# Kernel tuning notes

Measured on AMD Instinct MI355X. Metric: run time of the kernel, lower is better.

## Reference

```python
import jax, jax.numpy as jnp
import numpy as np

N_NODES = 25000
N_EDGES = 400000
EMBED_DIM = 128
NUM_HEADS = 8
D_K = EMBED_DIM // NUM_HEADS


def setup_inputs() -> dict:
    key = jax.random.key(0)
    ks = jax.random.split(key, 8)
    sc = 1.0 / np.sqrt(EMBED_DIM)
    return {
        "x": jax.random.normal(ks[0], (N_NODES, EMBED_DIM), jnp.float32),
        "edge_index": jax.random.randint(ks[1], (2, N_EDGES), 0, N_NODES),
        "attn_bias": jax.random.normal(ks[2], (N_EDGES, NUM_HEADS), jnp.float32),
        "Wq": jax.random.normal(ks[3], (EMBED_DIM, EMBED_DIM), jnp.float32) * sc,
        "bq": jnp.zeros((EMBED_DIM,), jnp.float32),
        "Wk": jax.random.normal(ks[4], (EMBED_DIM, EMBED_DIM), jnp.float32) * sc,
        "bk": jnp.zeros((EMBED_DIM,), jnp.float32),
        "Wv": jax.random.normal(ks[5], (EMBED_DIM, EMBED_DIM), jnp.float32) * sc,
        "bv": jnp.zeros((EMBED_DIM,), jnp.float32),
        "Wo": jax.random.normal(ks[6], (EMBED_DIM, EMBED_DIM), jnp.float32) * sc,
        "bo": jnp.zeros((EMBED_DIM,), jnp.float32),
    }


def reference(x, edge_index, attn_bias, Wq, bq, Wk, bk, Wv, bv, Wo, bo):
    N = x.shape[0]
    E = edge_index.shape[1]
    H, dk = NUM_HEADS, D_K
    scale = 1.0 / np.sqrt(dk).astype(np.float32)
    dst = edge_index[0]  # query/aggregation node per edge
    src = edge_index[1]  # key/value node per edge

    # project at node level (as torch: linear(x)[index]), then gather per edge
    q = (x @ Wq.T + bq)[dst].reshape(E, H, dk)
    k = (x @ Wk.T + bk)[src].reshape(E, H, dk)
    v = (x @ Wv.T + bv)[src].reshape(E, H, dk)

    logits = scale * jnp.sum(q * k, axis=2) + attn_bias  # [E, H]

    # segment softmax over edges grouped by destination node
    m = jax.ops.segment_max(logits, dst, num_segments=N)     # [N, H]
    e = jnp.exp(logits - m[dst])                              # [E, H]
    z = jax.ops.segment_sum(e, dst, num_segments=N)           # [N, H]
    scores = e / z[dst]                                       # [E, H]

    agg = jax.ops.segment_sum(scores[..., None] * v, dst, num_segments=N)  # [N, H, dk]
    out = agg.reshape(N, H * dk) @ Wo.T + bo                   # [N, embed_dim]
    return out, logits[..., None]
```

## Files before the change

kernel.cpp:

```cpp
#include <hip/hip_runtime.h>
#include <math.h>

#define N_NODES 25000
#define N_EDGES 400000
#define EMBED   128
#define HEADS   8
#define DK      16
#define MAXDEG  96
#define NX (N_NODES * 128)
#define GBLK 391
#define SCAT_BLK 391
#define TOT_BLK (3 * GBLK + SCAT_BLK)

typedef __attribute__((ext_vector_type(8))) short bf16x8;
typedef __attribute__((ext_vector_type(4))) float f32x4;
typedef unsigned int uint;
typedef unsigned short ushort;

__device__ inline uint pack2_bf16(float a, float b) {
    union { float f; uint u; } ua, ub;
    ua.f = a; ub.f = b;
    uint ra = (ua.u + 0x7FFFu + ((ua.u >> 16) & 1u)) >> 16;
    uint rb = (ub.u + 0x7FFFu + ((ub.u >> 16) & 1u)) >> 16;
    return (ra & 0xFFFFu) | (rb << 16);
}
__device__ inline ushort cvt_bf16(float a) {
    union { float f; uint u; } ua; ua.f = a;
    return (ushort)((ua.u + 0x7FFFu + ((ua.u >> 16) & 1u)) >> 16);
}
__device__ inline float bf16_lo(uint u) {
    union { uint u; float f; } x; x.u = u << 16; return x.f;
}
__device__ inline float bf16_hi(uint u) {
    union { uint u; float f; } x; x.u = u & 0xFFFF0000u; return x.f;
}

__global__ __launch_bounds__(256) void prep(
    const float* __restrict__ Wq, const float* __restrict__ Wk,
    const float* __restrict__ Wv, const float* __restrict__ Wo,
    ushort* __restrict__ wb, int* __restrict__ deg)
{
    int i = blockIdx.x * 256 + threadIdx.x;
    if (i < N_NODES) deg[i] = 0;
    if (i < 32768) {
        int j = i * 2;
        const float* src = (j < 16384) ? Wq + j
                         : (j < 32768) ? Wk + (j - 16384)
                         : (j < 49152) ? Wv + (j - 32768)
                         :               Wo + (j - 49152);
        float2 v = *reinterpret_cast<const float2*>(src);
        reinterpret_cast<uint*>(wb)[i] = pack2_bf16(v.x, v.y);
    }
}

__global__ __launch_bounds__(256) void gemm_qkv_scatter(
    const float* __restrict__ x, const ushort* __restrict__ Wall,
    const float* __restrict__ bq, const float* __restrict__ bk,
    const float* __restrict__ bv,
    ushort* __restrict__ Qb, ushort* __restrict__ Kb, ushort* __restrict__ Vb,
    const int* __restrict__ ei, int* __restrict__ deg, int2* __restrict__ csr2)
{
    const int bx = blockIdx.x;
    if ((bx & 3) == 3) {
        int t = (bx >> 2) * 256 + threadIdx.x;
        int e = t * 4;
        if (e < N_EDGES) {
            int4 d = *reinterpret_cast<const int4*>(ei + e);
            int4 s = *reinterpret_cast<const int4*>(ei + N_EDGES + e);
            int p0 = atomicAdd(&deg[d.x], 1);
            if (p0 < MAXDEG) csr2[d.x * MAXDEG + p0] = make_int2(e, s.x);
            int p1 = atomicAdd(&deg[d.y], 1);
            if (p1 < MAXDEG) csr2[d.y * MAXDEG + p1] = make_int2(e + 1, s.y);
            int p2 = atomicAdd(&deg[d.z], 1);
            if (p2 < MAXDEG) csr2[d.z * MAXDEG + p2] = make_int2(e + 2, s.z);
            int p3 = atomicAdd(&deg[d.w], 1);
            if (p3 < MAXDEG) csr2[d.w * MAXDEG + p3] = make_int2(e + 3, s.w);
        }
        return;
    }

    const int gi    = (bx >> 2) * 3 + (bx & 3);
    const int which = gi / GBLK;
    const int mb    = gi - which * GBLK;
    const ushort* W = Wall + which * 16384;
    const float* bias = (which == 0) ? bq : (which == 1) ? bk : bv;
    ushort* C = (which == 0) ? Qb : (which == 1) ? Kb : Vb;

    const int lane = threadIdx.x & 63;
    const int wave = threadIdx.x >> 6;
    const int ml   = lane & 15;
    const int quad = lane >> 4;
    const int m0   = mb * 64 + wave * 16;

    int arow = m0 + ml; if (arow >= N_NODES) arow = N_NODES - 1;
    const float* xp = x + arow * 128 + quad * 8;

    bf16x8 af[4];
#pragma unroll
    for (int ks = 0; ks < 4; ++ks) {
        float4 a0 = *reinterpret_cast<const float4*>(xp + ks * 32);
        float4 a1 = *reinterpret_cast<const float4*>(xp + ks * 32 + 4);
        uint* u = reinterpret_cast<uint*>(&af[ks]);
        u[0] = pack2_bf16(a0.x, a0.y); u[1] = pack2_bf16(a0.z, a0.w);
        u[2] = pack2_bf16(a1.x, a1.y); u[3] = pack2_bf16(a1.z, a1.w);
    }

    f32x4 acc[8];
#pragma unroll
    for (int ct = 0; ct < 8; ++ct) acc[ct] = (f32x4){0.f, 0.f, 0.f, 0.f};

#pragma unroll
    for (int ks = 0; ks < 4; ++ks) {
#pragma unroll
        for (int ct = 0; ct < 8; ++ct) {
            bf16x8 bf = *reinterpret_cast<const bf16x8*>(
                W + (ct * 16 + ml) * 128 + ks * 32 + quad * 8);
            acc[ct] = __builtin_amdgcn_mfma_f32_16x16x32_bf16(af[ks], bf, acc[ct], 0, 0, 0);
        }
    }

#pragma unroll
    for (int ct = 0; ct < 8; ++ct) {
        int col = ct * 16 + ml;
        float b = bias[col];
#pragma unroll
        for (int r = 0; r < 4; ++r) {
            int row = m0 + quad * 4 + r;
            if (row < N_NODES)
                C[row * 128 + col] = cvt_bf16(acc[ct][r] + b);
        }
    }
}

__global__ __launch_bounds__(256) void fused_attn_out(
    const ushort* __restrict__ Q2, const ushort* __restrict__ K2,
    const ushort* __restrict__ V2,
    const float* __restrict__ attn_bias,
    const int* __restrict__ deg, const int2* __restrict__ csr2,
    const ushort* __restrict__ Wo2, const float* __restrict__ bo,
    float* __restrict__ logits, float* __restrict__ out)
{
    __shared__ ushort agg_sh[16 * 136];

    const int tid  = threadIdx.x;
    const int lane = tid & 63;
    const int wid  = tid >> 6;
    const int n0 = blockIdx.x * 4;
    const int n  = n0 + wid;
    int dg = deg[n]; if (dg > MAXDEG) dg = MAXDEG;
    const int start = n * MAXDEG;
    const int h  = lane & 7;
    const int es = lane >> 3;
    const int ml   = lane & 15;
    const int quad = lane >> 4;

    if (tid < 204)
        *reinterpret_cast<uint4*>(reinterpret_cast<char*>(agg_sh) + 1088 + tid * 16) =
            make_uint4(0u, 0u, 0u, 0u);

    const uint4* Qu4 = reinterpret_cast<const uint4*>(Q2);
    const uint4* Ku4 = reinterpret_cast<const uint4*>(K2);
    const uint4* Vu4 = reinterpret_cast<const uint4*>(V2);

    uint4 qa = Qu4[n * 16 + h * 2];
    uint4 qb = Qu4[n * 16 + h * 2 + 1];
    float qf[16];
    {
        uint qq[8] = {qa.x, qa.y, qa.z, qa.w, qb.x, qb.y, qb.z, qb.w};
#pragma unroll
        for (int j = 0; j < 8; ++j) {
            qf[2 * j]     = bf16_lo(qq[j]);
            qf[2 * j + 1] = bf16_hi(qq[j]);
        }
    }

    float acc[16];
#pragma unroll
    for (int j = 0; j < 16; ++j) acc[j] = 0.f;
    float z = 0.f;

    if (dg > 0) {
        int2 ep = csr2[start + (es < dg ? es : dg - 1)];
        for (int base = 0; base < dg; base += 8) {
            int e = ep.x, s = ep.y;
            bool valid = (base + es) < dg;

            uint4 k0 = Ku4[s * 16 + h * 2];
            uint4 k1 = Ku4[s * 16 + h * 2 + 1];
            uint4 v0 = Vu4[s * 16 + h * 2];
            uint4 v1 = Vu4[s * 16 + h * 2 + 1];
            float bias = attn_bias[e * 8 + h];

            int nb = base + 8;
            if (nb < dg) {
                int t2 = nb + es; if (t2 >= dg) t2 = dg - 1;
                ep = csr2[start + t2];
            }

            uint kk[8] = {k0.x, k0.y, k0.z, k0.w, k1.x, k1.y, k1.z, k1.w};
            float d = 0.f;
#pragma unroll
            for (int j = 0; j < 8; ++j)
                d += qf[2 * j] * bf16_lo(kk[j]) + qf[2 * j + 1] * bf16_hi(kk[j]);

            float l = 0.25f * d + bias;
            float p = 0.f;
            if (valid) {
                __builtin_nontemporal_store(l, &logits[e * 8 + h]);
                p = __expf(l);
            }
            z += p;

            uint vv[8] = {v0.x, v0.y, v0.z, v0.w, v1.x, v1.y, v1.z, v1.w};
#pragma unroll
            for (int j = 0; j < 8; ++j) {
                acc[2 * j]     += p * bf16_lo(vv[j]);
                acc[2 * j + 1] += p * bf16_hi(vv[j]);
            }
        }
    }

    {
        int bit = (lane >> 5) & 1;
#pragma unroll
        for (int j = 0; j < 8; ++j) {
            float send = bit ? acc[j] : acc[j + 8];
            float keep = bit ? acc[j + 8] : acc[j];
            acc[j] = keep + __shfl_xor(send, 32, 64);
        }
        bit = (lane >> 4) & 1;
#pragma unroll
        for (int j = 0; j < 4; ++j) {
            float send = bit ? acc[j] : acc[j + 4];
            float keep = bit ? acc[j + 4] : acc[j];
            acc[j] = keep + __shfl_xor(send, 16, 64);
        }
        bit = (lane >> 3) & 1;
#pragma unroll
        for (int j = 0; j < 2; ++j) {
            float send = bit ? acc[j] : acc[j + 2];
            float keep = bit ? acc[j + 2] : acc[j];
            acc[j] = keep + __shfl_xor(send, 8, 64);
        }
    }
    z += __shfl_xor(z, 8, 64);
    z += __shfl_xor(z, 16, 64);
    z += __shfl_xor(z, 32, 64);

    float inv = (z > 0.f) ? 1.f / z : 0.f;
    int d_off = ((lane >> 5) & 1) * 8 + ((lane >> 4) & 1) * 4 + ((lane >> 3) & 1) * 2;
    *reinterpret_cast<uint*>(reinterpret_cast<char*>(agg_sh) + wid * 272 +
                             (h * 16 + d_off) * 2) =
        pack2_bf16(acc[0] * inv, acc[1] * inv);

    __syncthreads();

    {
        bf16x8 af[4];
#pragma unroll
        for (int ks = 0; ks < 4; ++ks)
            af[ks] = *reinterpret_cast<const bf16x8*>(
                reinterpret_cast<char*>(agg_sh) + ml * 272 + ks * 64 + quad * 16);

        f32x4 oacc[2];
        oacc[0] = (f32x4){0.f, 0.f, 0.f, 0.f};
        oacc[1] = (f32x4){0.f, 0.f, 0.f, 0.f};

#pragma unroll
        for (int ks = 0; ks < 4; ++ks) {
#pragma unroll
            for (int c = 0; c < 2; ++c) {
                bf16x8 bf = *reinterpret_cast<const bf16x8*>(
                    Wo2 + ((wid * 2 + c) * 16 + ml) * 128 + ks * 32 + quad * 8);
                oacc[c] = __builtin_amdgcn_mfma_f32_16x16x32_bf16(af[ks], bf, oacc[c], 0, 0, 0);
            }
        }

        if (quad == 0) {
#pragma unroll
            for (int c = 0; c < 2; ++c) {
                int col = (wid * 2 + c) * 16 + ml;
                float b = bo[col];
#pragma unroll
                for (int r = 0; r < 4; ++r)
                    out[(n0 + r) * 128 + col] = oacc[c][r] + b;
            }
        }
    }
}

extern "C" void kernel_launch(void* const* d_in, const int* in_sizes, int n_in,
                              void* d_out, int out_size, void* d_ws, size_t ws_size,
                              hipStream_t stream)
{
    const float* x         = (const float*)d_in[0];
    const int*   ei        = (const int*)  d_in[1];
    const float* attn_bias = (const float*)d_in[2];
    const float* Wq = (const float*)d_in[3];
    const float* bq = (const float*)d_in[4];
    const float* Wk = (const float*)d_in[5];
    const float* bk = (const float*)d_in[6];
    const float* Wv = (const float*)d_in[7];
    const float* bv = (const float*)d_in[8];
    const float* Wo = (const float*)d_in[9];
    const float* bo = (const float*)d_in[10];

    float* out    = (float*)d_out;
    float* logits = out + N_NODES * EMBED;

    ushort* wb   = (ushort*)d_ws;
    ushort* Qb   = wb + 4 * 16384;
    ushort* Kb   = Qb + NX;
    ushort* Vb   = Kb + NX;
    int* deg     = (int*)(Vb + NX);
    int2* csr2   = (int2*)(deg + N_NODES);

    prep<<<128, 256, 0, stream>>>(Wq, Wk, Wv, Wo, wb, deg);

    gemm_qkv_scatter<<<TOT_BLK, 256, 0, stream>>>(
        x, wb, bq, bk, bv, Qb, Kb, Vb, ei, deg, csr2);

    fused_attn_out<<<N_NODES / 4, 256, 0, stream>>>(Qb, Kb, Vb, attn_bias,
                                                    deg, csr2, wb + 3 * 16384,
                                                    bo, logits, out);
}
```

Baseline: 186.5 us.

## Merge three kernel launches into one persistent cooperative kernel with grid syncs

Replaces the prep, QKV GEMM/scatter and attention launches with one cooperative persistent kernel that grid-strides over virtual blocks and separates the phases with grid.sync(). The grid is sized from the occupancy query. The goal is to remove launch gaps and tail effects between kernels. In exchange it adds grid-wide barrier cost, caps occupancy through the grid size, and falls back to the old three launches if the cooperative launch fails.

```diff
diff --git a/kernel.cpp b/kernel.cpp
--- a/kernel.cpp
+++ b/kernel.cpp
@@ -1,4 +1,5 @@
 #include <hip/hip_runtime.h>
+#include <hip/hip_cooperative_groups.h>
 #include <math.h>
 
 #define N_NODES 25000
@@ -11,6 +12,9 @@
 #define GBLK 391
 #define SCAT_BLK 391
 #define TOT_BLK (3 * GBLK + SCAT_BLK)
+#define ATTN_VB (N_NODES / 4)
+
+namespace cg = cooperative_groups;
 
 typedef __attribute__((ext_vector_type(8))) short bf16x8;
 typedef __attribute__((ext_vector_type(4))) float f32x4;
@@ -33,6 +37,257 @@
 }
 __device__ inline float bf16_hi(uint u) {
     union { uint u; float f; } x; x.u = u & 0xFFFF0000u; return x.f;
+}
+
+__global__ __launch_bounds__(256, 4) void fused_all(
+    const float* __restrict__ x, const int* __restrict__ ei,
+    const float* __restrict__ attn_bias,
+    const float* __restrict__ Wq, const float* __restrict__ bq,
+    const float* __restrict__ Wk, const float* __restrict__ bk,
+    const float* __restrict__ Wv, const float* __restrict__ bv,
+    const float* __restrict__ Wo, const float* __restrict__ bo,
+    ushort* __restrict__ wb,
+    ushort* __restrict__ Qb, ushort* __restrict__ Kb, ushort* __restrict__ Vb,
+    int* __restrict__ deg, int2* __restrict__ csr2,
+    float* __restrict__ logits, float* __restrict__ out)
+{
+    __shared__ ushort agg_sh[16 * 136];
+    cg::grid_group grid = cg::this_grid();
+    const int tid = threadIdx.x;
+    const int nb  = gridDim.x;
+    const int lane = tid & 63;
+    const int wid  = tid >> 6;
+    const int ml   = lane & 15;
+    const int quad = lane >> 4;
+
+    for (int vb = blockIdx.x; vb < 226; vb += nb) {
+        if (vb < 128) {
+            int i = vb * 256 + tid;
+            int j = i * 2;
+            const float* src = (j < 16384) ? Wq + j
+                             : (j < 32768) ? Wk + (j - 16384)
+                             : (j < 49152) ? Wv + (j - 32768)
+                             :               Wo + (j - 49152);
+            float2 v = *reinterpret_cast<const float2*>(src);
+            reinterpret_cast<uint*>(wb)[i] = pack2_bf16(v.x, v.y);
+        } else {
+            int i = (vb - 128) * 256 + tid;
+            if (i < N_NODES) deg[i] = 0;
+        }
+    }
+    grid.sync();
+
+    for (int vb = blockIdx.x; vb < TOT_BLK; vb += nb) {
+        if ((vb & 3) == 3) {
+            int t = (vb >> 2) * 256 + tid;
+            int e = t * 4;
+            if (e < N_EDGES) {
+                int4 d = *reinterpret_cast<const int4*>(ei + e);
+                int4 s = *reinterpret_cast<const int4*>(ei + N_EDGES + e);
+                int p0 = atomicAdd(&deg[d.x], 1);
+                if (p0 < MAXDEG) csr2[d.x * MAXDEG + p0] = make_int2(e, s.x);
+                int p1 = atomicAdd(&deg[d.y], 1);
+                if (p1 < MAXDEG) csr2[d.y * MAXDEG + p1] = make_int2(e + 1, s.y);
+                int p2 = atomicAdd(&deg[d.z], 1);
+                if (p2 < MAXDEG) csr2[d.z * MAXDEG + p2] = make_int2(e + 2, s.z);
+                int p3 = atomicAdd(&deg[d.w], 1);
+                if (p3 < MAXDEG) csr2[d.w * MAXDEG + p3] = make_int2(e + 3, s.w);
+            }
+        } else {
+            const int gi    = (vb >> 2) * 3 + (vb & 3);
+            const int which = gi / GBLK;
+            const int mb    = gi - which * GBLK;
+            const ushort* W = wb + which * 16384;
+            const float* bias = (which == 0) ? bq : (which == 1) ? bk : bv;
+            ushort* C = (which == 0) ? Qb : (which == 1) ? Kb : Vb;
+            const int m0 = mb * 64 + wid * 16;
+
+            int arow = m0 + ml; if (arow >= N_NODES) arow = N_NODES - 1;
+            const float* xp = x + arow * 128 + quad * 8;
+
+            bf16x8 af[4];
+#pragma unroll
+            for (int ks = 0; ks < 4; ++ks) {
+                float4 a0 = *reinterpret_cast<const float4*>(xp + ks * 32);
+                float4 a1 = *reinterpret_cast<const float4*>(xp + ks * 32 + 4);
+                uint* u = reinterpret_cast<uint*>(&af[ks]);
+                u[0] = pack2_bf16(a0.x, a0.y); u[1] = pack2_bf16(a0.z, a0.w);
+                u[2] = pack2_bf16(a1.x, a1.y); u[3] = pack2_bf16(a1.z, a1.w);
+            }
+
+            f32x4 acc[8];
+#pragma unroll
+            for (int ct = 0; ct < 8; ++ct) acc[ct] = (f32x4){0.f, 0.f, 0.f, 0.f};
+
+#pragma unroll
+            for (int ks = 0; ks < 4; ++ks) {
+#pragma unroll
+                for (int ct = 0; ct < 8; ++ct) {
+                    bf16x8 bf = *reinterpret_cast<const bf16x8*>(
+                        W + (ct * 16 + ml) * 128 + ks * 32 + quad * 8);
+                    acc[ct] = __builtin_amdgcn_mfma_f32_16x16x32_bf16(af[ks], bf, acc[ct], 0, 0, 0);
+                }
+            }
+
+#pragma unroll
+            for (int ct = 0; ct < 8; ++ct) {
+                int col = ct * 16 + ml;
+                float b = bias[col];
+#pragma unroll
+                for (int r = 0; r < 4; ++r) {
+                    int row = m0 + quad * 4 + r;
+                    if (row < N_NODES)
+                        C[row * 128 + col] = cvt_bf16(acc[ct][r] + b);
+                }
+            }
+        }
+    }
+    grid.sync();
+
+    const int h  = lane & 7;
+    const int es = lane >> 3;
+    const uint4* Qu4 = reinterpret_cast<const uint4*>(Qb);
+    const uint4* Ku4 = reinterpret_cast<const uint4*>(Kb);
+    const uint4* Vu4 = reinterpret_cast<const uint4*>(Vb);
+    const ushort* Wo2 = wb + 3 * 16384;
+
+    if (tid < 204)
+        *reinterpret_cast<uint4*>(reinterpret_cast<char*>(agg_sh) + 1088 + tid * 16) =
+            make_uint4(0u, 0u, 0u, 0u);
+
+    for (int vb = blockIdx.x; vb < ATTN_VB; vb += nb) {
+        const int n0 = vb * 4;
+        const int n  = n0 + wid;
+        int dg = deg[n]; if (dg > MAXDEG) dg = MAXDEG;
+        const int start = n * MAXDEG;
+
+        uint4 qa = Qu4[n * 16 + h * 2];
+        uint4 qb2 = Qu4[n * 16 + h * 2 + 1];
+        float qf[16];
+        {
+            uint qq[8] = {qa.x, qa.y, qa.z, qa.w, qb2.x, qb2.y, qb2.z, qb2.w};
+#pragma unroll
+            for (int j = 0; j < 8; ++j) {
+                qf[2 * j]     = bf16_lo(qq[j]);
+                qf[2 * j + 1] = bf16_hi(qq[j]);
+            }
+        }
+
+        float acc[16];
+#pragma unroll
+        for (int j = 0; j < 16; ++j) acc[j] = 0.f;
+        float z = 0.f;
+
+        if (dg > 0) {
+            int2 ep = csr2[start + (es < dg ? es : dg - 1)];
+            for (int base = 0; base < dg; base += 8) {
+                int e = ep.x, s = ep.y;
+                bool valid = (base + es) < dg;
+
+                uint4 k0 = Ku4[s * 16 + h * 2];
+                uint4 k1 = Ku4[s * 16 + h * 2 + 1];
+                uint4 v0 = Vu4[s * 16 + h * 2];
+                uint4 v1 = Vu4[s * 16 + h * 2 + 1];
+                float bias = attn_bias[e * 8 + h];
+
+                int nbatch = base + 8;
+                if (nbatch < dg) {
+                    int t2 = nbatch + es; if (t2 >= dg) t2 = dg - 1;
+                    ep = csr2[start + t2];
+                }
+
+                uint kk[8] = {k0.x, k0.y, k0.z, k0.w, k1.x, k1.y, k1.z, k1.w};
+                float d = 0.f;
+#pragma unroll
+                for (int j = 0; j < 8; ++j)
+                    d += qf[2 * j] * bf16_lo(kk[j]) + qf[2 * j + 1] * bf16_hi(kk[j]);
+
+                float l = 0.25f * d + bias;
+                float p = 0.f;
+                if (valid) {
+                    __builtin_nontemporal_store(l, &logits[e * 8 + h]);
+                    p = __expf(l);
+                }
+                z += p;
+
+                uint vv[8] = {v0.x, v0.y, v0.z, v0.w, v1.x, v1.y, v1.z, v1.w};
+#pragma unroll
+                for (int j = 0; j < 8; ++j) {
+                    acc[2 * j]     += p * bf16_lo(vv[j]);
+                    acc[2 * j + 1] += p * bf16_hi(vv[j]);
+                }
+            }
+        }
+
+        {
+            int bit = (lane >> 5) & 1;
+#pragma unroll
+            for (int j = 0; j < 8; ++j) {
+                float send = bit ? acc[j] : acc[j + 8];
+                float keep = bit ? acc[j + 8] : acc[j];
+                acc[j] = keep + __shfl_xor(send, 32, 64);
+            }
+            bit = (lane >> 4) & 1;
+#pragma unroll
+            for (int j = 0; j < 4; ++j) {
+                float send = bit ? acc[j] : acc[j + 4];
+                float keep = bit ? acc[j + 4] : acc[j];
+                acc[j] = keep + __shfl_xor(send, 16, 64);
+            }
+            bit = (lane >> 3) & 1;
+#pragma unroll
+            for (int j = 0; j < 2; ++j) {
+                float send = bit ? acc[j] : acc[j + 2];
+                float keep = bit ? acc[j + 2] : acc[j];
+                acc[j] = keep + __shfl_xor(send, 8, 64);
+            }
+        }
+        z += __shfl_xor(z, 8, 64);
+        z += __shfl_xor(z, 16, 64);
+        z += __shfl_xor(z, 32, 64);
+
+        float inv = (z > 0.f) ? 1.f / z : 0.f;
+        int d_off = ((lane >> 5) & 1) * 8 + ((lane >> 4) & 1) * 4 + ((lane >> 3) & 1) * 2;
+        *reinterpret_cast<uint*>(reinterpret_cast<char*>(agg_sh) + wid * 272 +
+                                 (h * 16 + d_off) * 2) =
+            pack2_bf16(acc[0] * inv, acc[1] * inv);
+
+        __syncthreads();
+
+        {
+            bf16x8 af[4];
+#pragma unroll
+            for (int ks = 0; ks < 4; ++ks)
+                af[ks] = *reinterpret_cast<const bf16x8*>(
+                    reinterpret_cast<char*>(agg_sh) + ml * 272 + ks * 64 + quad * 16);
+
+            f32x4 oacc[2];
+            oacc[0] = (f32x4){0.f, 0.f, 0.f, 0.f};
+            oacc[1] = (f32x4){0.f, 0.f, 0.f, 0.f};
+
+#pragma unroll
+            for (int ks = 0; ks < 4; ++ks) {
+#pragma unroll
+                for (int c = 0; c < 2; ++c) {
+                    bf16x8 bf = *reinterpret_cast<const bf16x8*>(
+                        Wo2 + ((wid * 2 + c) * 16 + ml) * 128 + ks * 32 + quad * 8);
+                    oacc[c] = __builtin_amdgcn_mfma_f32_16x16x32_bf16(af[ks], bf, oacc[c], 0, 0, 0);
+                }
+            }
+
+            if (quad == 0) {
+#pragma unroll
+                for (int c = 0; c < 2; ++c) {
+                    int col = (wid * 2 + c) * 16 + ml;
+                    float b = bo[col];
+#pragma unroll
+                    for (int r = 0; r < 4; ++r)
+                        out[(n0 + r) * 128 + col] = oacc[c][r] + b;
+                }
+            }
+        }
+        __syncthreads();
+    }
 }
 
 __global__ __launch_bounds__(256) void prep(
@@ -78,7 +333,6 @@
         }
         return;
     }
-
     const int gi    = (bx >> 2) * 3 + (bx & 3);
     const int which = gi / GBLK;
     const int mb    = gi - which * GBLK;
@@ -315,12 +569,33 @@
     int* deg     = (int*)(Vb + NX);
     int2* csr2   = (int2*)(deg + N_NODES);
 
-    prep<<<128, 256, 0, stream>>>(Wq, Wk, Wv, Wo, wb, deg);
-
-    gemm_qkv_scatter<<<TOT_BLK, 256, 0, stream>>>(
-        x, wb, bq, bk, bv, Qb, Kb, Vb, ei, deg, csr2);
-
-    fused_attn_out<<<N_NODES / 4, 256, 0, stream>>>(Qb, Kb, Vb, attn_bias,
-                                                    deg, csr2, wb + 3 * 16384,
-                                                    bo, logits, out);
-}
+    int per_cu = 4;
+    if (hipOccupancyMaxActiveBlocksPerMultiprocessor(
+            &per_cu, reinterpret_cast<const void*>(fused_all), 256, 0) != hipSuccess
+        || per_cu < 1)
+        per_cu = 4;
+    if (per_cu > 8) per_cu = 8;
+    int grid = per_cu * 256;
+    if (grid > 2048) grid = 2048;
+
+    void* kargs[] = {
+        (void*)&x, (void*)&ei, (void*)&attn_bias,
+        (void*)&Wq, (void*)&bq, (void*)&Wk, (void*)&bk,
+        (void*)&Wv, (void*)&bv, (void*)&Wo, (void*)&bo,
+        (void*)&wb, (void*)&Qb, (void*)&Kb, (void*)&Vb,
+        (void*)&deg, (void*)&csr2, (void*)&logits, (void*)&out
+    };
+
+    hipError_t err = hipLaunchCooperativeKernel(
+        reinterpret_cast<const void*>(fused_all),
+        dim3(grid), dim3(256), kargs, 0, stream);
+
+    if (err != hipSuccess) {
+        prep<<<128, 256, 0, stream>>>(Wq, Wk, Wv, Wo, wb, deg);
+        gemm_qkv_scatter<<<TOT_BLK, 256, 0, stream>>>(
+            x, wb, bq, bk, bv, Qb, Kb, Vb, ei, deg, csr2);
+        fused_attn_out<<<N_NODES / 4, 256, 0, stream>>>(Qb, Kb, Vb, attn_bias,
+                                                        deg, csr2, wb + 3 * 16384,
+                                                        bo, logits, out);
+    }
+}
```

Result: slower. 317.2 us (+70.1%).
